# Optimization experiments

Hardware: AMD Instinct MI355X
Metric: run time of the kernel (lower is better)

The kernel has to match this reference:

```python
import jax, jax.numpy as jnp
import numpy as np

B, N, E, F_IN, F_OUT = 4, 50000, 800000, 128, 128


def setup_inputs() -> dict:
    key = jax.random.key(0)
    k1, k2, k3, k4, k5 = jax.random.split(key, 5)
    x = jax.random.normal(k1, (B, N, F_IN), dtype=jnp.float32)
    # nn.Linear(in, out, bias=False) weight: [out_features, in_features]
    W = jax.random.normal(k2, (F_OUT, F_IN), dtype=jnp.float32) * (1.0 / np.sqrt(F_IN))
    edge_row = jax.random.randint(k3, (E,), 0, N, dtype=jnp.int64)
    edge_col = jax.random.randint(k4, (E,), 0, N, dtype=jnp.int64)
    edge_vals = jax.random.uniform(k5, (E,), dtype=jnp.float32)
    return {"x": x, "W": W, "edge_row": edge_row, "edge_col": edge_col, "edge_vals": edge_vals}


def reference(x, W, edge_row, edge_col, edge_vals):
    # x: [B, N, F_in]; linear projection (no bias): h = x @ W^T -> [B, N, F_out]
    h = jnp.einsum('bnf,of->bno', x, W)

    # SpMM: out[r] = sum_{edges (r,c)} A[r,c] * h[c], vmapped over batch
    def spmm(hb):  # hb: [N, F_out]
        msg = hb[edge_col] * edge_vals[:, None]  # [E, F_out]
        return jax.ops.segment_sum(msg, edge_row, num_segments=N)

    return jax.vmap(spmm)(h)  # [B, N, F_out]
```

## Files before the change

### kernel.cpp

```cpp
#include <hip/hip_runtime.h>
#include <stdint.h>

#define NB 4
#define NN 50000
#define NE 800000
#define NF 128

#define NBLK 49
#define LDK 72
#define LDT 136

typedef __attribute__((ext_vector_type(8))) short  bfrag;
typedef __attribute__((ext_vector_type(4))) float  ffrag;
typedef __attribute__((ext_vector_type(4))) short  short4v;
typedef __attribute__((ext_vector_type(4))) float  f32x4;

__device__ inline unsigned short f2bf(float f) {
    unsigned int u = __builtin_bit_cast(unsigned int, f);
    u += 0x7fffu + ((u >> 16) & 1u);
    return (unsigned short)(u >> 16);
}
__device__ inline float bflo(unsigned int u) { return __builtin_bit_cast(float, u << 16); }
__device__ inline float bfhi(unsigned int u) { return __builtin_bit_cast(float, u & 0xffff0000u); }

__global__ __launch_bounds__(256) void gemm_kernel(
    const float* __restrict__ x,
    const float* __restrict__ W,
    unsigned short* __restrict__ h,
    const int* __restrict__ erow,
    int* __restrict__ cnt,
    int M)
{
    __shared__ short smem[2 * 128 * LDK];
    short* xs  = smem;
    short* wsh = smem + 128 * LDK;

    const int tid  = threadIdx.x;

    for (int e = blockIdx.x * 256 + tid; e < NE; e += gridDim.x * 256)
        atomicAdd(&cnt[erow[e]], 1);

    const int w    = tid >> 6;
    const int lane = tid & 63;
    const int wr   = w >> 1;
    const int wc   = w & 1;
    const int q    = lane >> 4;
    const int l15  = lane & 15;
    const int m0   = blockIdx.x * 128;

    ffrag acc[4][4];
#pragma unroll
    for (int i = 0; i < 4; ++i)
#pragma unroll
        for (int j = 0; j < 4; ++j) acc[i][j] = (ffrag)0.f;

    for (int kc = 0; kc < 2; ++kc) {
        const int c = kc * 64;
        __syncthreads();
#pragma unroll
        for (int it = 0; it < 8; ++it) {
            int linear = it * 256 + tid;
            int r  = linear >> 4;
            int k4 = linear & 15;

            float4 wv = *(const float4*)(W + (size_t)r * NF + c + k4 * 4);
            short4v wsv;
            wsv[0] = (short)f2bf(wv.x); wsv[1] = (short)f2bf(wv.y);
            wsv[2] = (short)f2bf(wv.z); wsv[3] = (short)f2bf(wv.w);
            *(short4v*)&wsh[r * LDK + k4 * 4] = wsv;

            int gr = m0 + r;
            float4 xv = make_float4(0.f, 0.f, 0.f, 0.f);
            if (gr < M) xv = *(const float4*)(x + (size_t)gr * NF + c + k4 * 4);
            short4v xsv;
            xsv[0] = (short)f2bf(xv.x); xsv[1] = (short)f2bf(xv.y);
            xsv[2] = (short)f2bf(xv.z); xsv[3] = (short)f2bf(xv.w);
            *(short4v*)&xs[r * LDK + k4 * 4] = xsv;
        }
        __syncthreads();

#pragma unroll
        for (int ks = 0; ks < 2; ++ks) {
            const int ko = ks * 32 + q * 8;
            bfrag a[4], b[4];
#pragma unroll
            for (int i = 0; i < 4; ++i)
                a[i] = *(const bfrag*)&xs[(wr * 64 + i * 16 + l15) * LDK + ko];
#pragma unroll
            for (int j = 0; j < 4; ++j)
                b[j] = *(const bfrag*)&wsh[(wc * 64 + j * 16 + l15) * LDK + ko];
#pragma unroll
            for (int i = 0; i < 4; ++i)
#pragma unroll
                for (int j = 0; j < 4; ++j)
                    acc[i][j] = __builtin_amdgcn_mfma_f32_16x16x32_bf16(
                        a[i], b[j], acc[i][j], 0, 0, 0);
        }
    }

    __syncthreads();
    short* tile = smem;
#pragma unroll
    for (int i = 0; i < 4; ++i)
#pragma unroll
        for (int reg = 0; reg < 4; ++reg) {
            int row = wr * 64 + i * 16 + q * 4 + reg;
#pragma unroll
            for (int j = 0; j < 4; ++j)
                tile[row * LDT + wc * 64 + j * 16 + l15] =
                    (short)f2bf(acc[i][j][reg]);
        }
    __syncthreads();
#pragma unroll
    for (int it = 0; it < 8; ++it) {
        int row = it * 16 + (tid >> 4);
        int m   = m0 + row;
        if (m < M) {
            int n  = m % NN;
            int bb = m / NN;
            uint4 v = *(const uint4*)&tile[row * LDT + (tid & 15) * 8];
            *(uint4*)(h + ((size_t)n * NB + bb) * NF + (tid & 15) * 8) = v;
        }
    }
}

__global__ __launch_bounds__(1024) void scan1_kernel(
    const int* __restrict__ cnt, int* __restrict__ rs, int* __restrict__ bsum)
{
    __shared__ int wsum[16];
    const int tid  = threadIdx.x;
    const int lane = tid & 63;
    const int wid  = tid >> 6;
    const int i    = blockIdx.x * 1024 + tid;

    int v = (i < NN) ? cnt[i] : 0;
    int incl = v;
#pragma unroll
    for (int off = 1; off < 64; off <<= 1) {
        int t = __shfl_up(incl, off, 64);
        if (lane >= off) incl += t;
    }
    if (lane == 63) wsum[wid] = incl;
    __syncthreads();
    int woff = 0;
    for (int ww = 0; ww < wid; ++ww) woff += wsum[ww];
    if (i < NN) rs[i] = woff + incl - v;
    if (tid == 0) {
        int tot = 0;
        for (int ww = 0; ww < 16; ++ww) tot += wsum[ww];
        bsum[blockIdx.x] = tot;
    }
}

__global__ void scan2_kernel(int* __restrict__ bsum)
{
    int lane = threadIdx.x;
    int v = (lane < NBLK) ? bsum[lane] : 0;
    int incl = v;
#pragma unroll
    for (int off = 1; off < 64; off <<= 1) {
        int t = __shfl_up(incl, off, 64);
        if (lane >= off) incl += t;
    }
    if (lane < NBLK) bsum[lane] = incl - v;
}

__global__ void scatter_kernel(const int* __restrict__ row,
                               const int* __restrict__ col,
                               const float* __restrict__ val,
                               const int* __restrict__ rs,
                               const int* __restrict__ bsum,
                               int* __restrict__ cursor,
                               uint2* __restrict__ cv_s)
{
    int e = blockIdx.x * 256 + threadIdx.x;
    if (e < NE) {
        int r   = row[e];
        int p   = atomicAdd(&cursor[r], 1);
        int dst = rs[r] + bsum[r >> 10] + p;
        uint2 cv;
        cv.x = (unsigned)col[e];
        cv.y = __builtin_bit_cast(unsigned, val[e]);
        cv_s[dst] = cv;
    }
}

__global__ __launch_bounds__(256) void spmm_kernel(
    const unsigned short* __restrict__ h,
    const int* __restrict__ rs,
    const int* __restrict__ bsum,
    const uint2* __restrict__ cv_s,
    float* __restrict__ out)
{
    const int w    = threadIdx.x >> 6;
    const int lane = threadIdx.x & 63;
    int r = blockIdx.x * 4 + w;
    if (r >= NN) return;
    r = __builtin_amdgcn_readfirstlane(r);

    const int s = rs[r] + bsum[r >> 10];
    const int e = (r + 1 == NN) ? NE : rs[r + 1] + bsum[(r + 1) >> 10];
    const int b    = lane >> 4;
    const int loff = b * NF + (lane & 15) * 8;

    float acc[8];
#pragma unroll
    for (int k = 0; k < 8; ++k) acc[k] = 0.f;

    for (int base = s; base < e; base += 64) {
        const int n = min(64, e - base);
        unsigned long long cvp = 0ull;
        if (lane < n)
            cvp = __builtin_nontemporal_load(
                      (const unsigned long long*)(cv_s + base + lane));
        const int cvx = (int)(unsigned)(cvp & 0xffffffffull);
        const int cvy = (int)(unsigned)(cvp >> 32);

        const int n4 = (n + 3) & ~3;
        for (int i = 0; i < n4; i += 4) {
            const unsigned c0 = (unsigned)__builtin_amdgcn_readlane(cvx, i);
            const unsigned c1 = (unsigned)__builtin_amdgcn_readlane(cvx, i + 1);
            const unsigned c2 = (unsigned)__builtin_amdgcn_readlane(cvx, i + 2);
            const unsigned c3 = (unsigned)__builtin_amdgcn_readlane(cvx, i + 3);
            const uint4 q0 = *(const uint4*)(h + (size_t)c0 * (NB * NF) + loff);
            const uint4 q1 = *(const uint4*)(h + (size_t)c1 * (NB * NF) + loff);
            const uint4 q2 = *(const uint4*)(h + (size_t)c2 * (NB * NF) + loff);
            const uint4 q3 = *(const uint4*)(h + (size_t)c3 * (NB * NF) + loff);
            const float v0 = __builtin_bit_cast(
                float, __builtin_amdgcn_readlane(cvy, i));
            const float v1 = __builtin_bit_cast(
                float, __builtin_amdgcn_readlane(cvy, i + 1));
            const float v2 = __builtin_bit_cast(
                float, __builtin_amdgcn_readlane(cvy, i + 2));
            const float v3 = __builtin_bit_cast(
                float, __builtin_amdgcn_readlane(cvy, i + 3));

            acc[0] += v0 * bflo(q0.x); acc[1] += v0 * bfhi(q0.x);
            acc[2] += v0 * bflo(q0.y); acc[3] += v0 * bfhi(q0.y);
            acc[4] += v0 * bflo(q0.z); acc[5] += v0 * bfhi(q0.z);
            acc[6] += v0 * bflo(q0.w); acc[7] += v0 * bfhi(q0.w);
            acc[0] += v1 * bflo(q1.x); acc[1] += v1 * bfhi(q1.x);
            acc[2] += v1 * bflo(q1.y); acc[3] += v1 * bfhi(q1.y);
            acc[4] += v1 * bflo(q1.z); acc[5] += v1 * bfhi(q1.z);
            acc[6] += v1 * bflo(q1.w); acc[7] += v1 * bfhi(q1.w);
            acc[0] += v2 * bflo(q2.x); acc[1] += v2 * bfhi(q2.x);
            acc[2] += v2 * bflo(q2.y); acc[3] += v2 * bfhi(q2.y);
            acc[4] += v2 * bflo(q2.z); acc[5] += v2 * bfhi(q2.z);
            acc[6] += v2 * bflo(q2.w); acc[7] += v2 * bfhi(q2.w);
            acc[0] += v3 * bflo(q3.x); acc[1] += v3 * bfhi(q3.x);
            acc[2] += v3 * bflo(q3.y); acc[3] += v3 * bfhi(q3.y);
            acc[4] += v3 * bflo(q3.z); acc[5] += v3 * bfhi(q3.z);
            acc[6] += v3 * bflo(q3.w); acc[7] += v3 * bfhi(q3.w);
        }
    }

    float* op = out + ((size_t)b * NN + r) * NF + (lane & 15) * 8;
    f32x4 o0 = {acc[0], acc[1], acc[2], acc[3]};
    f32x4 o1 = {acc[4], acc[5], acc[6], acc[7]};
    __builtin_nontemporal_store(o0, (f32x4*)op);
    __builtin_nontemporal_store(o1, (f32x4*)(op + 4));
}

extern "C" void kernel_launch(void* const* d_in, const int* in_sizes, int n_in,
                              void* d_out, int out_size, void* d_ws, size_t ws_size,
                              hipStream_t stream)
{
    const float* x    = (const float*)d_in[0];
    const float* W    = (const float*)d_in[1];
    const int*   erow = (const int*)d_in[2];
    const int*   ecol = (const int*)d_in[3];
    const float* ev   = (const float*)d_in[4];
    float*       out  = (float*)d_out;

    char*  ws  = (char*)d_ws;
    size_t off = 0;
    auto alloc = [&](size_t bytes) -> void* {
        void* p = ws + off;
        off += (bytes + 255) & ~(size_t)255;
        return p;
    };
    unsigned short* h = (unsigned short*)alloc((size_t)NN * NB * NF * sizeof(unsigned short));
    int*   rs     = (int*)  alloc((size_t)(NN + 1) * sizeof(int));
    int*   cnt    = (int*)  alloc((size_t)2 * NN * sizeof(int));
    int*   cursor = cnt + NN;
    int*   bsum   = (int*)  alloc((size_t)64 * sizeof(int));
    uint2* cv_s   = (uint2*)alloc((size_t)NE * sizeof(uint2));

    hipMemsetAsync(cnt, 0, (size_t)2 * NN * sizeof(int), stream);

    const int M = NB * NN;
    gemm_kernel<<<(M + 127) / 128, 256, 0, stream>>>(x, W, h, erow, cnt, M);

    scan1_kernel<<<NBLK, 1024, 0, stream>>>(cnt, rs, bsum);
    scan2_kernel<<<1, 64, 0, stream>>>(bsum);
    scatter_kernel<<<(NE + 255) / 256, 256, 0, stream>>>(erow, ecol, ev, rs,
                                                         bsum, cursor, cv_s);

    spmm_kernel<<<(NN + 3) / 4, 256, 0, stream>>>(h, rs, bsum, cv_s, out);
}
```

Measured before the change: 402.1 us.

## Load x fragments directly from global in GEMM and stage full W once

The GEMM kernel no longer stages x tiles through shared memory. Each wave reads its 32 rows of x straight from global into MFMA A-fragments, converting to bf16 in registers, while the whole bf16 W matrix is staged in LDS once per block. This removes the per-chunk LDS round trip and two barriers per K chunk, but the x loads are strided 32-byte reads per lane rather than coalesced tile loads. The SpMM output stores also switch from nontemporal to ordinary stores.

```diff
diff --git a/kernel.cpp b/kernel.cpp
--- a/kernel.cpp
+++ b/kernel.cpp
@@ -7,8 +7,7 @@
 #define NF 128
 
 #define NBLK 49
-#define LDK 72
-#define LDT 136
+#define LDW 136
 
 typedef __attribute__((ext_vector_type(8))) short  bfrag;
 typedef __attribute__((ext_vector_type(4))) float  ffrag;
@@ -31,94 +30,90 @@
     int* __restrict__ cnt,
     int M)
 {
-    __shared__ short smem[2 * 128 * LDK];
-    short* xs  = smem;
-    short* wsh = smem + 128 * LDK;
-
-    const int tid  = threadIdx.x;
+    __shared__ short wsh[128 * LDW];
+
+    const int tid = threadIdx.x;
 
     for (int e = blockIdx.x * 256 + tid; e < NE; e += gridDim.x * 256)
         atomicAdd(&cnt[erow[e]], 1);
 
+#pragma unroll
+    for (int it = 0; it < 16; ++it) {
+        int idx = it * 256 + tid;
+        int r   = idx >> 5;
+        int c4  = idx & 31;
+        float4 wv = *(const float4*)(W + (size_t)r * NF + c4 * 4);
+        short4v wsv;
+        wsv[0] = (short)f2bf(wv.x); wsv[1] = (short)f2bf(wv.y);
+        wsv[2] = (short)f2bf(wv.z); wsv[3] = (short)f2bf(wv.w);
+        *(short4v*)&wsh[r * LDW + c4 * 4] = wsv;
+    }
+    __syncthreads();
+
     const int w    = tid >> 6;
     const int lane = tid & 63;
-    const int wr   = w >> 1;
-    const int wc   = w & 1;
     const int q    = lane >> 4;
     const int l15  = lane & 15;
-    const int m0   = blockIdx.x * 128;
-
-    ffrag acc[4][4];
-#pragma unroll
-    for (int i = 0; i < 4; ++i)
-#pragma unroll
-        for (int j = 0; j < 4; ++j) acc[i][j] = (ffrag)0.f;
-
-    for (int kc = 0; kc < 2; ++kc) {
-        const int c = kc * 64;
-        __syncthreads();
-#pragma unroll
-        for (int it = 0; it < 8; ++it) {
-            int linear = it * 256 + tid;
-            int r  = linear >> 4;
-            int k4 = linear & 15;
-
-            float4 wv = *(const float4*)(W + (size_t)r * NF + c + k4 * 4);
-            short4v wsv;
-            wsv[0] = (short)f2bf(wv.x); wsv[1] = (short)f2bf(wv.y);
-            wsv[2] = (short)f2bf(wv.z); wsv[3] = (short)f2bf(wv.w);
-            *(short4v*)&wsh[r * LDK + k4 * 4] = wsv;
-
-            int gr = m0 + r;
-            float4 xv = make_float4(0.f, 0.f, 0.f, 0.f);
-            if (gr < M) xv = *(const float4*)(x + (size_t)gr * NF + c + k4 * 4);
-            short4v xsv;
-            xsv[0] = (short)f2bf(xv.x); xsv[1] = (short)f2bf(xv.y);
-            xsv[2] = (short)f2bf(xv.z); xsv[3] = (short)f2bf(xv.w);
-            *(short4v*)&xs[r * LDK + k4 * 4] = xsv;
-        }
-        __syncthreads();
-
-#pragma unroll
-        for (int ks = 0; ks < 2; ++ks) {
-            const int ko = ks * 32 + q * 8;
-            bfrag a[4], b[4];
-#pragma unroll
-            for (int i = 0; i < 4; ++i)
-                a[i] = *(const bfrag*)&xs[(wr * 64 + i * 16 + l15) * LDK + ko];
-#pragma unroll
-            for (int j = 0; j < 4; ++j)
-                b[j] = *(const bfrag*)&wsh[(wc * 64 + j * 16 + l15) * LDK + ko];
-#pragma unroll
-            for (int i = 0; i < 4; ++i)
-#pragma unroll
-                for (int j = 0; j < 4; ++j)
-                    acc[i][j] = __builtin_amdgcn_mfma_f32_16x16x32_bf16(
-                        a[i], b[j], acc[i][j], 0, 0, 0);
-        }
-    }
-
-    __syncthreads();
-    short* tile = smem;
-#pragma unroll
-    for (int i = 0; i < 4; ++i)
+    const int r0   = blockIdx.x * 128 + w * 32;
+
+    const float* xp[2];
+#pragma unroll
+    for (int i = 0; i < 2; ++i) {
+        int gr = r0 + i * 16 + l15;
+        gr = gr < M ? gr : M - 1;
+        xp[i] = x + (size_t)gr * NF + q * 8;
+    }
+
+    ffrag acc[2][8];
+#pragma unroll
+    for (int i = 0; i < 2; ++i)
+#pragma unroll
+        for (int j = 0; j < 8; ++j) acc[i][j] = (ffrag)0.f;
+
+#pragma unroll 2
+    for (int kc = 0; kc < 4; ++kc) {
+        bfrag a[2];
+#pragma unroll
+        for (int i = 0; i < 2; ++i) {
+            float4 u0 = *(const float4*)(xp[i] + kc * 32);
+            float4 u1 = *(const float4*)(xp[i] + kc * 32 + 4);
+            bfrag t;
+            t[0] = (short)f2bf(u0.x); t[1] = (short)f2bf(u0.y);
+            t[2] = (short)f2bf(u0.z); t[3] = (short)f2bf(u0.w);
+            t[4] = (short)f2bf(u1.x); t[5] = (short)f2bf(u1.y);
+            t[6] = (short)f2bf(u1.z); t[7] = (short)f2bf(u1.w);
+            a[i] = t;
+        }
+#pragma unroll
+        for (int j = 0; j < 8; ++j) {
+            bfrag b = *(const bfrag*)&wsh[(j * 16 + l15) * LDW + kc * 32 + q * 8];
+            acc[0][j] = __builtin_amdgcn_mfma_f32_16x16x32_bf16(
+                a[0], b, acc[0][j], 0, 0, 0);
+            acc[1][j] = __builtin_amdgcn_mfma_f32_16x16x32_bf16(
+                a[1], b, acc[1][j], 0, 0, 0);
+        }
+    }
+
+    __syncthreads();
+    short* tile = wsh;
+#pragma unroll
+    for (int i = 0; i < 2; ++i)
 #pragma unroll
         for (int reg = 0; reg < 4; ++reg) {
-            int row = wr * 64 + i * 16 + q * 4 + reg;
-#pragma unroll
-            for (int j = 0; j < 4; ++j)
-                tile[row * LDT + wc * 64 + j * 16 + l15] =
-                    (short)f2bf(acc[i][j][reg]);
+            int row = w * 32 + i * 16 + q * 4 + reg;
+#pragma unroll
+            for (int j = 0; j < 8; ++j)
+                tile[row * LDW + j * 16 + l15] = (short)f2bf(acc[i][j][reg]);
         }
     __syncthreads();
 #pragma unroll
     for (int it = 0; it < 8; ++it) {
         int row = it * 16 + (tid >> 4);
-        int m   = m0 + row;
+        int m   = blockIdx.x * 128 + row;
         if (m < M) {
             int n  = m % NN;
             int bb = m / NN;
-            uint4 v = *(const uint4*)&tile[row * LDT + (tid & 15) * 8];
+            uint4 v = *(const uint4*)&tile[row * LDW + (tid & 15) * 8];
             *(uint4*)(h + ((size_t)n * NB + bb) * NF + (tid & 15) * 8) = v;
         }
     }
@@ -255,10 +250,8 @@
     }
 
     float* op = out + ((size_t)b * NN + r) * NF + (lane & 15) * 8;
-    f32x4 o0 = {acc[0], acc[1], acc[2], acc[3]};
-    f32x4 o1 = {acc[4], acc[5], acc[6], acc[7]};
-    __builtin_nontemporal_store(o0, (f32x4*)op);
-    __builtin_nontemporal_store(o1, (f32x4*)(op + 4));
+    *(float4*)op       = make_float4(acc[0], acc[1], acc[2], acc[3]);
+    *(float4*)(op + 4) = make_float4(acc[4], acc[5], acc[6], acc[7]);
 }
 
 extern "C" void kernel_launch(void* const* d_in, const int* in_sizes, int n_in,
```

Measured after the change: 378.5 us. -5.9%, faster.
